# Optimization experiments

Measured on AMD Instinct MI355X. Metric: run time of the kernel, lower is better.

Reference implementation:

```python
import jax, jax.numpy as jnp
import numpy as np

B, NMAX, D, NUM = 1024, 128, 256, 4
EPS = 1e-8
NEG = -1e9


def segment_softmax(logits, seg):
    # torch_geometric-style softmax over ragged segments. logits: (T,)
    m = jax.ops.segment_max(logits, seg, num_segments=B)
    e = jnp.exp(logits - m[seg])
    s = jax.ops.segment_sum(e, seg, num_segments=B)
    return e / (s[seg] + 1e-16)


def to_dense(v, seg, pos):
    # scatter ragged rows into (B, NMAX, ...) dense batch
    return jnp.zeros((B, NMAX) + v.shape[1:], v.dtype).at[seg, pos].set(v)


def uot_badmm(x, q0d, maskf, a1, a2, a3, rho):
    # Bregman-ADMM solver for entropic unbalanced OT (f_method='badmm-e').
    # x: (B,N,D) cost (to be maximized); q0d, maskf: (B,N,1); a1,a2,a3,rho: (NUM,)
    log_p0 = jnp.full((B, 1, D), -jnp.log(float(D)), x.dtype)  # uniform dim prior
    log_q0 = jnp.log(q0d + EPS)                                # (B,N,1)
    log_t = log_q0 + log_p0                                    # T init = q0 p0^T
    log_s = log_t
    log_mu = log_p0
    log_eta = log_q0
    z = jnp.zeros_like(x)
    z1 = jnp.zeros_like(log_p0)
    z2 = jnp.zeros_like(log_q0)
    neg = (1.0 - maskf) * NEG  # exclude padded rows from N-axis softmax
    for k in range(NUM):
        r, b1, b2, b3 = rho[k], a1[k], a2[k], a3[k]
        # T-update: rows (over D) sum to eta
        y = (x - z + r * log_s) / (b2 + r)
        log_t = log_eta + jax.nn.log_softmax(y, axis=2)
        # S-update: columns (over N) sum to mu, masked
        y = (z + r * log_t) / (b1 + r) + neg
        log_s = log_mu + jax.nn.log_softmax(y, axis=1)
        # unbalanced marginal updates (KL to priors, weight a3)
        log_mu = (b3 * log_p0 - z1 + r * jax.nn.logsumexp(log_s, axis=1, keepdims=True)) / (b3 + r)
        log_eta = (b3 * log_q0 - z2 + r * jax.nn.logsumexp(log_t, axis=2, keepdims=True)) / (b3 + r)
        # dual ascent
        t = jnp.exp(log_t) * maskf
        s = jnp.exp(log_s) * maskf
        z = z + r * (t - s)
        z1 = z1 + r * (jnp.exp(log_mu) - jnp.sum(s, axis=1, keepdims=True))
        z2 = z2 + r * (jnp.exp(log_eta) - jnp.sum(t, axis=2, keepdims=True)) * maskf
    return jnp.exp(log_t) * maskf


def setup_inputs() -> dict:
    rng = np.random.default_rng(0)
    lengths = rng.integers(NMAX // 2, NMAX + 1, size=B)
    lengths[0] = NMAX  # ensure max size present
    batch = jnp.asarray(np.repeat(np.arange(B), lengths), dtype=jnp.int32)
    total = int(lengths.sum())
    ks = jax.random.split(jax.random.key(0), 8)
    x = jax.random.normal(ks[0], (total, D), jnp.float32)
    W1 = jax.random.normal(ks[1], (2 * D, D), jnp.float32) / np.float32(np.sqrt(D))
    W2 = jax.random.normal(ks[2], (1, 2 * D), jnp.float32) / np.float32(np.sqrt(2 * D))
    rho = 0.1 * jax.random.normal(ks[3], (NUM,), jnp.float32)
    a1 = 0.1 * jax.random.normal(ks[4], (NUM,), jnp.float32)
    a2 = 0.1 * jax.random.normal(ks[5], (NUM,), jnp.float32)
    a3 = 0.1 * jax.random.normal(ks[6], (NUM,), jnp.float32)
    return {"x": x, "batch": batch, "W1": W1, "W2": W2, "rho": rho, "a1": a1, "a2": a2, "a3": a3}


def reference(x, batch, W1, W2, rho, a1, a2, a3):
    # attention-based sample prior q0 (q0 != 'fixed' branch)
    h = jnp.tanh(x @ W1.T)          # (T, 2D)
    logits = (h @ W2.T)[:, 0]       # (T,)
    q0 = segment_softmax(logits, batch)[:, None]  # (T, 1)
    # ragged -> dense batch (to_dense_batch)
    counts = jax.ops.segment_sum(jnp.ones_like(batch), batch, num_segments=B)
    starts = jnp.cumsum(counts) - counts
    pos = jnp.arange(batch.shape[0]) - starts[batch]
    xd = to_dense(x, batch, pos)    # (B, NMAX, D)
    q0d = to_dense(q0, batch, pos)  # (B, NMAX, 1)
    mask = to_dense(jnp.ones((batch.shape[0], 1), x.dtype), batch, pos)  # (B, NMAX, 1)
    trans = uot_badmm(xd, q0d, mask,
                      jax.nn.softplus(a1), jax.nn.softplus(a2),
                      jax.nn.softplus(a3), jax.nn.softplus(rho))
    frot = D * xd * trans * mask    # (B, NMAX, D)
    return jnp.sum(frot, axis=1)    # (B, D)
```

## Files before the change

kernel.cpp:

```cpp
#include <hip/hip_runtime.h>
#include <math.h>

#define BB   1024
#define DD   256
#define LOGD 5.5451774444795624753f

typedef __attribute__((ext_vector_type(8))) short short8;
typedef __attribute__((ext_vector_type(4))) float f32x4;

__device__ __forceinline__ float wave_sum(float v){
  #pragma unroll
  for (int off=32; off>0; off>>=1) v += __shfl_xor(v, off, 64);
  return v;
}
__device__ __forceinline__ float wave_max(float v){
  #pragma unroll
  for (int off=32; off>0; off>>=1) v = fmaxf(v, __shfl_xor(v, off, 64));
  return v;
}
__device__ __forceinline__ float fast_tanh(float x){
  return 1.0f - 2.0f/(__expf(2.0f*x)+1.0f);
}
__device__ __forceinline__ unsigned short f2bf(float f){
  unsigned int u = __float_as_uint(f);
  unsigned int r = u + 0x7FFFu + ((u >> 16) & 1u);
  return (unsigned short)(r >> 16);
}
__device__ __forceinline__ float rfl(float x){
  return __uint_as_float(__builtin_amdgcn_readfirstlane(__float_as_uint(x)));
}
__device__ __forceinline__ int encq(float v){
  return (int)(fmaxf(v, -63.0f)*512.0f - 0.5f);
}
__device__ __forceinline__ float decq(int q16){
  return (float)q16 * (1.0f/512.0f);
}
__device__ __forceinline__ int zenc(float z){
  float t = fmaf(z, 4096.0f, 12582912.0f);
  return __float_as_int(t) - 0x4B400000;
}
__device__ __forceinline__ float zdec(int q){
  return (float)q * (1.0f/4096.0f);
}
__device__ __forceinline__ int upk16(unsigned v, int hi){
  return hi ? ((int)v >> 16) : (((int)(v << 16)) >> 16);
}

__global__ void k_pre(const float* __restrict__ W1, unsigned short* __restrict__ w1b,
                      const int* __restrict__ batch, int T, int* __restrict__ starts,
                      const float* __restrict__ rho, const float* __restrict__ a1,
                      const float* __restrict__ a2, const float* __restrict__ a3,
                      float* __restrict__ P)
{
  const int blk = blockIdx.x, tid = threadIdx.x;
  if (blk < 64){
    const int t = blk*256 + tid;
    #pragma unroll
    for (int i=0;i<2;i++){
      const int idx = (t*2 + i)*4;
      const float4 v = *(const float4*)(W1 + idx);
      *(ushort4*)(w1b + idx) = make_ushort4(f2bf(v.x), f2bf(v.y), f2bf(v.z), f2bf(v.w));
    }
  } else if (blk < 69){
    const int b = (blk-64)*256 + tid;
    if (b <= BB){
      int lo = 0, hi = T;
      while (lo < hi){ int mid = (lo+hi)>>1; if (batch[mid] < b) lo = mid+1; else hi = mid; }
      starts[b] = lo;
    }
  } else if (tid == 0){
    float lm = -LOGD, z1 = 0.f;
    for (int k=0;k<4;k++){
      float r  = log1pf(expf(rho[k]));
      float b1 = log1pf(expf(a1[k]));
      float b2 = log1pf(expf(a2[k]));
      float b3 = log1pf(expf(a3[k]));
      P[k]    = r;
      P[4+k]  = 1.f/(b1+r);
      P[8+k]  = 1.f/(b2+r);
      P[12+k] = lm;
      P[16+k] = b3;
      P[20+k] = 1.f/(b3+r);
      float lmn = (b3*(-LOGD) - z1 + r*lm)/(b3+r);
      z1 += r*(expf(lmn)-expf(lm));
      lm = lmn;
    }
  }
}

#define LPW 72
__global__ __launch_bounds__(512, 2) void k_mlp(
    const float* __restrict__ x, const unsigned short* __restrict__ w1b,
    const float* __restrict__ W2, float* __restrict__ logits, int T)
{
  __shared__ unsigned short Xs[128*LPW];
  __shared__ unsigned short Ws[128*LPW];
  __shared__ float lred[128];
  const int by = blockIdx.x;
  const int bx = blockIdx.y;
  const int tid = threadIdx.x;
  if (tid < 128) lred[tid] = 0.f;

  const int l = tid & 63;
  const int w = tid >> 6;
  const int wm = w >> 2;
  const int wn = w & 3;
  const int lr = l & 15, quad = l >> 4;
  const int srow = tid >> 2;
  const int sseg = tid & 3;
  const int wrow = tid >> 3;
  const int wseg = tid & 7;

  f32x4 acc[4][2];
  #pragma unroll
  for (int mi=0;mi<4;mi++)
    #pragma unroll
    for (int ni=0;ni<2;ni++) acc[mi][ni] = (f32x4){0.f,0.f,0.f,0.f};

  for (int kt=0; kt<4; kt++){
    const int k0 = kt*64;
    {
      const int grow = bx*128 + srow;
      #pragma unroll
      for (int i=0;i<4;i++){
        float4 v = make_float4(0.f,0.f,0.f,0.f);
        if (grow < T) v = *(const float4*)(x + (size_t)grow*DD + k0 + sseg*16 + i*4);
        *(ushort4*)&Xs[srow*LPW + sseg*16 + i*4] =
            make_ushort4(f2bf(v.x), f2bf(v.y), f2bf(v.z), f2bf(v.w));
      }
    }
    #pragma unroll
    for (int h=0; h<2; h++){
      const int r = h*64 + wrow;
      *(short8*)&Ws[r*LPW + wseg*8] =
          *(const short8*)(w1b + (size_t)(by*128 + r)*DD + k0 + wseg*8);
    }
    __syncthreads();
    #pragma unroll
    for (int ks=0; ks<2; ks++){
      short8 afr[4], bfr[2];
      #pragma unroll
      for (int mi=0;mi<4;mi++)
        afr[mi] = *(const short8*)&Xs[(wm*64 + mi*16 + lr)*LPW + ks*32 + quad*8];
      #pragma unroll
      for (int ni=0;ni<2;ni++)
        bfr[ni] = *(const short8*)&Ws[(wn*32 + ni*16 + lr)*LPW + ks*32 + quad*8];
      #pragma unroll
      for (int mi=0;mi<4;mi++)
        #pragma unroll
        for (int ni=0;ni<2;ni++)
          acc[mi][ni] = __builtin_amdgcn_mfma_f32_16x16x32_bf16(afr[mi], bfr[ni], acc[mi][ni], 0, 0, 0);
    }
    __syncthreads();
  }

  float w2v[2];
  #pragma unroll
  for (int ni=0;ni<2;ni++) w2v[ni] = W2[by*128 + wn*32 + ni*16 + lr];
  #pragma unroll
  for (int mi=0;mi<4;mi++){
    float p[4];
    #pragma unroll
    for (int v=0; v<4; v++){
      p[v] = fast_tanh(acc[mi][0][v])*w2v[0] + fast_tanh(acc[mi][1][v])*w2v[1];
      #pragma unroll
      for (int off=1; off<16; off<<=1) p[v] += __shfl_xor(p[v], off, 64);
    }
    if (lr == 0){
      #pragma unroll
      for (int v=0; v<4; v++)
        atomicAdd(&lred[wm*64 + mi*16 + quad*4 + v], p[v]);
    }
  }
  __syncthreads();
  if (tid < 128){
    const int grow = bx*128 + tid;
    if (grow < T) atomicAdd(logits + grow, lred[tid]);
  }
}

__global__ __launch_bounds__(1024, 8) void k_solver(
    const float* __restrict__ x, const float* __restrict__ logits,
    const int* __restrict__ starts, const float* __restrict__ P,
    float* __restrict__ out)
{
  __shared__ __align__(16) unsigned short As[128*DD];
  __shared__ float red[16*DD];
  const int b = blockIdx.x;
  const int start = starts[b];
  const int len = starts[b+1] - start;
  const int tid = threadIdx.x;
  const int w = tid >> 6, l = tid & 63;
  const int n0 = w*8;
  int nv = len - n0; nv = nv < 0 ? 0 : (nv > 8 ? 8 : nv);

  const float r0=P[0], r1=P[1], r2=P[2], r3=P[3];
  const float i10=P[4], i11=P[5], i12=P[6];
  const float i20=P[8], i21=P[9], i22=P[10], i23=P[11];
  const float mu0=P[12], mu1=P[13], mu2=P[14];
  const float b30=P[16], b31=P[17], b32=P[18];
  const float e30=P[20], e31=P[21], e32=P[22];

  const float* lg = logits + start;
  float v0 = (l      < len) ? lg[l]    : -3.0e38f;
  float v1 = (l+64   < len) ? lg[l+64] : -3.0e38f;
  float sm = wave_max(fmaxf(v0,v1));
  float se0 = (l    < len) ? __expf(v0-sm) : 0.f;
  float se1 = (l+64 < len) ? __expf(v1-sm) : 0.f;
  float ssum = wave_sum(se0+se1);
  const float sinv = 1.f/(ssum + 1e-16f);
  const float esel = (n0 < 64) ? se0 : se1;

  float slq[8], eta[8], z2[8];
  uint2 zp[8];
  #pragma unroll
  for (int r=0;r<8;r++){
    const float ev = __shfl(esel, (n0+r)&63, 64);
    const float lqv = __logf(ev*sinv + 1e-8f);
    slq[r] = rfl(lqv);
    eta[r] = slq[r];
    z2[r]  = 0.f;
    zp[r].x = 0u; zp[r].y = 0u;
  }
  const int abase = (n0 << 8) + (l << 2);

  {
    float sp[4] = {0.f,0.f,0.f,0.f};
    #pragma unroll
    for (int r=0;r<8;r++){
      if (r < nv){
        const float* xp = x + (size_t)(start+n0+r)*DD + l;
        const float a0 = slq[r] - LOGD;
        float xv[4], y[4];
        #pragma unroll
        for (int j=0;j<4;j++) xv[j] = xp[64*j];
        float se = 0.f;
        #pragma unroll
        for (int j=0;j<4;j++){ y[j] = (xv[j] + r0*a0) * i20; se += __expf(y[j]); }
        se = wave_sum(se);
        const float off = eta[r] - __logf(se);
        int q[4];
        #pragma unroll
        for (int j=0;j<4;j++) q[j] = encq(off + y[j]);
        uint2 pk;
        pk.x = ((unsigned)q[0] & 0xffffu) | ((unsigned)q[1] << 16);
        pk.y = ((unsigned)q[2] & 0xffffu) | ((unsigned)q[3] << 16);
        *(uint2*)&As[abase + (r<<8)] = pk;
        #pragma unroll
        for (int j=0;j<4;j++) sp[j] += __expf((r0*decq(q[j])) * i10);
        const float en = (b30*slq[r] - z2[r] + r0*eta[r]) * e30;
        const float z2n = z2[r] + r0*(__expf(en) - __expf(eta[r]));
        z2[r] = rfl(z2n);
        eta[r] = rfl(en);
      }
    }
    #pragma unroll
    for (int j=0;j<4;j++) red[w*DD + l + 64*j] = sp[j];
  }
  __syncthreads();
  if (tid < DD){
    float s = 0.f;
    #pragma unroll
    for (int ww=0; ww<16; ww++) s += red[ww*DD + tid];
    red[tid] = __logf(s);
  }
  __syncthreads();

  #pragma unroll
  for (int k=1;k<3;k++){
    const float rkm = (k==1)? r0 : r1;
    const float ib1m= (k==1)? i10 : i11;
    const float mum = (k==1)? mu0 : mu1;
    const float rk  = (k==1)? r1 : r2;
    const float ib1k= (k==1)? i11 : i12;
    const float ib2k= (k==1)? i21 : i22;
    const float b3k = (k==1)? b31 : b32;
    const float e3k = (k==1)? e31 : e32;
    float lsc[4];
    #pragma unroll
    for (int j=0;j<4;j++) lsc[j] = red[l+64*j];
    __syncthreads();
    float sp[4] = {0.f,0.f,0.f,0.f};
    #pragma unroll
    for (int r=0;r<8;r++){
      if (r < nv){
        const float* xp = x + (size_t)(start+n0+r)*DD + l;
        float xv[4];
        #pragma unroll
        for (int j=0;j<4;j++) xv[j] = xp[64*j];
        const uint2 pk = *(const uint2*)&As[abase + (r<<8)];
        const uint2 zr = zp[r];
        float y[4], se = 0.f;
        int nq[4];
        #pragma unroll
        for (int j=0;j<4;j++){
          const int q16 = upk16((j<2)? pk.x : pk.y, j&1);
          const float lt  = decq(q16);
          float zf = zdec(upk16((j<2)? zr.x : zr.y, j&1));
          const float ys  = (zf + rkm*lt) * ib1m;
          const float lsn = mum + ys - lsc[j];
          zf += rkm*(__expf(lt) - __expf(lsn));
          nq[j] = zenc(zf);
          y[j] = (xv[j] - zdec(nq[j]) + rk*lsn) * ib2k;
          se += __expf(y[j]);
        }
        zp[r].x = ((unsigned)nq[0] & 0xffffu) | ((unsigned)nq[1] << 16);
        zp[r].y = ((unsigned)nq[2] & 0xffffu) | ((unsigned)nq[3] << 16);
        se = wave_sum(se);
        const float off = eta[r] - __logf(se);
        int q[4];
        #pragma unroll
        for (int j=0;j<4;j++) q[j] = encq(off + y[j]);
        uint2 npk;
        npk.x = ((unsigned)q[0] & 0xffffu) | ((unsigned)q[1] << 16);
        npk.y = ((unsigned)q[2] & 0xffffu) | ((unsigned)q[3] << 16);
        *(uint2*)&As[abase + (r<<8)] = npk;
        #pragma unroll
        for (int j=0;j<4;j++) sp[j] += __expf((zdec(nq[j]) + rk*decq(q[j])) * ib1k);
        const float en = (b3k*slq[r] - z2[r] + rk*eta[r]) * e3k;
        const float z2n = z2[r] + rk*(__expf(en) - __expf(eta[r]));
        z2[r] = rfl(z2n);
        eta[r] = rfl(en);
      }
    }
    #pragma unroll
    for (int j=0;j<4;j++) red[w*DD + l + 64*j] = sp[j];
    __syncthreads();
    if (tid < DD){
      float s = 0.f;
      #pragma unroll
      for (int ww=0; ww<16; ww++) s += red[ww*DD + tid];
      red[tid] = __logf(s);
    }
    __syncthreads();
  }

  {
    float lsc[4];
    #pragma unroll
    for (int j=0;j<4;j++) lsc[j] = red[l+64*j];
    __syncthreads();
    float op[4] = {0.f,0.f,0.f,0.f};
    #pragma unroll
    for (int r=0;r<8;r++){
      if (r < nv){
        const float* xp = x + (size_t)(start+n0+r)*DD + l;
        float xv[4];
        #pragma unroll
        for (int j=0;j<4;j++) xv[j] = xp[64*j];
        const uint2 pk = *(const uint2*)&As[abase + (r<<8)];
        const uint2 zr = zp[r];
        float ey[4], se = 0.f;
        #pragma unroll
        for (int j=0;j<4;j++){
          const int q16 = upk16((j<2)? pk.x : pk.y, j&1);
          const float lt  = decq(q16);
          float zf = zdec(upk16((j<2)? zr.x : zr.y, j&1));
          const float ys  = (zf + r2*lt) * i12;
          const float lsn = mu2 + ys - lsc[j];
          zf += r2*(__expf(lt) - __expf(lsn));
          const float yv = (xv[j] - zf + r3*lsn) * i23;
          ey[j] = __expf(yv);
          se += ey[j];
        }
        se = wave_sum(se);
        const float rs = __expf(eta[r]) / se;
        #pragma unroll
        for (int j=0;j<4;j++) op[j] += xv[j]*ey[j]*rs;
      }
    }
    #pragma unroll
    for (int j=0;j<4;j++) red[w*DD + l + 64*j] = op[j];
    __syncthreads();
    if (tid < DD){
      float s = 0.f;
      #pragma unroll
      for (int ww=0; ww<16; ww++) s += red[ww*DD + tid];
      out[(size_t)b*DD + tid] = 256.0f * s;
    }
  }
}

extern "C" void kernel_launch(void* const* d_in, const int* in_sizes, int n_in,
                              void* d_out, int out_size, void* d_ws, size_t ws_size,
                              hipStream_t stream) {
  const float* x    = (const float*)d_in[0];
  const int*   batch= (const int*)d_in[1];
  const float* W1   = (const float*)d_in[2];
  const float* W2   = (const float*)d_in[3];
  const float* rho  = (const float*)d_in[4];
  const float* a1   = (const float*)d_in[5];
  const float* a2   = (const float*)d_in[6];
  const float* a3   = (const float*)d_in[7];
  float* out = (float*)d_out;
  const int T = in_sizes[1];

  float* logits = (float*)d_ws;
  int*   starts = (int*)(logits + T);
  float* P      = (float*)(starts + 1028);
  unsigned short* w1b = (unsigned short*)(P + 32);

  k_pre<<<70, 256, 0, stream>>>(W1, w1b, batch, T, starts, rho, a1, a2, a3, P);
  hipMemsetAsync(logits, 0, (size_t)T*sizeof(float), stream);
  k_mlp<<<dim3(4, (T+127)/128), 512, 0, stream>>>(x, w1b, W2, logits, T);
  k_solver<<<BB, 1024, 0, stream>>>(x, logits, starts, P, out);
}
```

Measured before the change: 365.2 us.

## Halve solver block size, give each wave 16 rows, vectorize x loads

The solver kernel now runs 512 threads per block, so each wave owns 16 sample rows instead of 8. Each lane now takes a contiguous group of 4 columns, which lets x be read with one float4 load per row instead of four strided loads. Column log-sums are written to a separate shared buffer, which removes one barrier per iteration and halves the cross-wave reduction depth. In exchange, each thread holds twice as much per-row state in registers and each block has less parallelism.

```diff
diff --git a/kernel.cpp b/kernel.cpp
--- a/kernel.cpp
+++ b/kernel.cpp
@@ -179,20 +179,21 @@
   }
 }
 
-__global__ __launch_bounds__(1024, 8) void k_solver(
+__global__ __launch_bounds__(512, 4) void k_solver(
     const float* __restrict__ x, const float* __restrict__ logits,
     const int* __restrict__ starts, const float* __restrict__ P,
     float* __restrict__ out)
 {
   __shared__ __align__(16) unsigned short As[128*DD];
-  __shared__ float red[16*DD];
+  __shared__ float red[8*DD];
+  __shared__ float colv[DD];
   const int b = blockIdx.x;
   const int start = starts[b];
   const int len = starts[b+1] - start;
   const int tid = threadIdx.x;
   const int w = tid >> 6, l = tid & 63;
-  const int n0 = w*8;
-  int nv = len - n0; nv = nv < 0 ? 0 : (nv > 8 ? 8 : nv);
+  const int n0 = w*16;
+  int nv = len - n0; nv = nv < 0 ? 0 : (nv > 16 ? 16 : nv);
 
   const float r0=P[0], r1=P[1], r2=P[2], r3=P[3];
   const float i10=P[4], i11=P[5], i12=P[6];
@@ -211,10 +212,10 @@
   const float sinv = 1.f/(ssum + 1e-16f);
   const float esel = (n0 < 64) ? se0 : se1;
 
-  float slq[8], eta[8], z2[8];
-  uint2 zp[8];
-  #pragma unroll
-  for (int r=0;r<8;r++){
+  float slq[16], eta[16], z2[16];
+  uint2 zp[16];
+  #pragma unroll
+  for (int r=0;r<16;r++){
     const float ev = __shfl(esel, (n0+r)&63, 64);
     const float lqv = __logf(ev*sinv + 1e-8f);
     slq[r] = rfl(lqv);
@@ -227,14 +228,12 @@
   {
     float sp[4] = {0.f,0.f,0.f,0.f};
     #pragma unroll
-    for (int r=0;r<8;r++){
+    for (int r=0;r<16;r++){
       if (r < nv){
-        const float* xp = x + (size_t)(start+n0+r)*DD + l;
+        const float4 xv4 = *(const float4*)(x + (size_t)(start+n0+r)*DD + 4*l);
+        const float xv[4] = {xv4.x, xv4.y, xv4.z, xv4.w};
         const float a0 = slq[r] - LOGD;
-        float xv[4], y[4];
-        #pragma unroll
-        for (int j=0;j<4;j++) xv[j] = xp[64*j];
-        float se = 0.f;
+        float y[4], se = 0.f;
         #pragma unroll
         for (int j=0;j<4;j++){ y[j] = (xv[j] + r0*a0) * i20; se += __expf(y[j]); }
         se = wave_sum(se);
@@ -255,14 +254,14 @@
       }
     }
     #pragma unroll
-    for (int j=0;j<4;j++) red[w*DD + l + 64*j] = sp[j];
+    for (int j=0;j<4;j++) red[w*DD + 4*l + j] = sp[j];
   }
   __syncthreads();
   if (tid < DD){
     float s = 0.f;
     #pragma unroll
-    for (int ww=0; ww<16; ww++) s += red[ww*DD + tid];
-    red[tid] = __logf(s);
+    for (int ww=0; ww<8; ww++) s += red[ww*DD + tid];
+    colv[tid] = __logf(s);
   }
   __syncthreads();
 
@@ -278,16 +277,13 @@
     const float e3k = (k==1)? e31 : e32;
     float lsc[4];
     #pragma unroll
-    for (int j=0;j<4;j++) lsc[j] = red[l+64*j];
-    __syncthreads();
+    for (int j=0;j<4;j++) lsc[j] = colv[4*l + j];
     float sp[4] = {0.f,0.f,0.f,0.f};
     #pragma unroll
-    for (int r=0;r<8;r++){
+    for (int r=0;r<16;r++){
       if (r < nv){
-        const float* xp = x + (size_t)(start+n0+r)*DD + l;
-        float xv[4];
-        #pragma unroll
-        for (int j=0;j<4;j++) xv[j] = xp[64*j];
+        const float4 xv4 = *(const float4*)(x + (size_t)(start+n0+r)*DD + 4*l);
+        const float xv[4] = {xv4.x, xv4.y, xv4.z, xv4.w};
         const uint2 pk = *(const uint2*)&As[abase + (r<<8)];
         const uint2 zr = zp[r];
         float y[4], se = 0.f;
@@ -324,13 +320,13 @@
       }
     }
     #pragma unroll
-    for (int j=0;j<4;j++) red[w*DD + l + 64*j] = sp[j];
+    for (int j=0;j<4;j++) red[w*DD + 4*l + j] = sp[j];
     __syncthreads();
     if (tid < DD){
       float s = 0.f;
       #pragma unroll
-      for (int ww=0; ww<16; ww++) s += red[ww*DD + tid];
-      red[tid] = __logf(s);
+      for (int ww=0; ww<8; ww++) s += red[ww*DD + tid];
+      colv[tid] = __logf(s);
     }
     __syncthreads();
   }
@@ -338,16 +334,13 @@
   {
     float lsc[4];
     #pragma unroll
-    for (int j=0;j<4;j++) lsc[j] = red[l+64*j];
-    __syncthreads();
+    for (int j=0;j<4;j++) lsc[j] = colv[4*l + j];
     float op[4] = {0.f,0.f,0.f,0.f};
     #pragma unroll
-    for (int r=0;r<8;r++){
+    for (int r=0;r<16;r++){
       if (r < nv){
-        const float* xp = x + (size_t)(start+n0+r)*DD + l;
-        float xv[4];
-        #pragma unroll
-        for (int j=0;j<4;j++) xv[j] = xp[64*j];
+        const float4 xv4 = *(const float4*)(x + (size_t)(start+n0+r)*DD + 4*l);
+        const float xv[4] = {xv4.x, xv4.y, xv4.z, xv4.w};
         const uint2 pk = *(const uint2*)&As[abase + (r<<8)];
         const uint2 zr = zp[r];
         float ey[4], se = 0.f;
@@ -370,12 +363,12 @@
       }
     }
     #pragma unroll
-    for (int j=0;j<4;j++) red[w*DD + l + 64*j] = op[j];
+    for (int j=0;j<4;j++) red[w*DD + 4*l + j] = op[j];
     __syncthreads();
     if (tid < DD){
       float s = 0.f;
       #pragma unroll
-      for (int ww=0; ww<16; ww++) s += red[ww*DD + tid];
+      for (int ww=0; ww<8; ww++) s += red[ww*DD + tid];
       out[(size_t)b*DD + tid] = 256.0f * s;
     }
   }
@@ -403,5 +396,5 @@
   k_pre<<<70, 256, 0, stream>>>(W1, w1b, batch, T, starts, rho, a1, a2, a3, P);
   hipMemsetAsync(logits, 0, (size_t)T*sizeof(float), stream);
   k_mlp<<<dim3(4, (T+127)/128), 512, 0, stream>>>(x, w1b, W2, logits, T);
-  k_solver<<<BB, 1024, 0, stream>>>(x, logits, starts, P, out);
-}
+  k_solver<<<BB, 512, 0, stream>>>(x, logits, starts, P, out);
+}
```

New measurement: 374.6 us. +2.6%, slower.
